# Performance work log

Measured on AMD Instinct MI355X. Metric: run time of the kernel, lower is better.

The kernel has to match this reference:

```python
import jax, jax.numpy as jnp
import numpy as np

B, X, Y, T = 8, 256, 256, 64   # input grid; T == fno_width
MODES = 16
PAD = 8
T_LOOKBACK = 16
SCALE = 1.0 / (T * T_LOOKBACK)  # 1/(fno_width*t_lookback)


def setup_inputs() -> dict:
    key = jax.random.key(0)
    ks = jax.random.split(key, 5)
    m = MODES
    x = jax.random.normal(ks[0], (B, X, Y, T), dtype=jnp.float32)
    w_tl = SCALE * jax.random.uniform(ks[1], (m, m, m), dtype=jnp.float32)
    w_tr = SCALE * jax.random.uniform(ks[2], (m, m, m), dtype=jnp.float32)
    w_bl = SCALE * jax.random.uniform(ks[3], (m, m, m), dtype=jnp.float32)
    w_br = SCALE * jax.random.uniform(ks[4], (m, m, m), dtype=jnp.float32)
    z = jnp.zeros((m, m, m), dtype=jnp.float32)
    return {"x": x, "w_tl": w_tl, "w_tr": w_tr, "w_bl": w_bl, "w_br": w_br,
            "b_tl": z, "b_tr": z, "b_bl": z, "b_br": z}


def reference(x, w_tl, w_tr, w_bl, w_br, b_tl, b_tr, b_bl, b_br):
    m, pad = MODES, PAD
    # pad all three non-batch dims
    xp = jnp.pad(x, ((0, 0), (pad, pad), (pad, pad), (pad, pad)))
    # tf: x = complex(x, x); x_ft = real(fft3d(x)) == Re(F(a)) - Im(F(a))
    xc = jax.lax.complex(xp, xp)
    x_ft = jnp.real(jnp.fft.fftn(xc, axes=(1, 2, 3)))
    # four corner mode blocks along axes 1,2; low modes along axis 3
    m_tl = x_ft[:, :m, :m, :m]
    m_tr = x_ft[:, -m:, :m, :m]
    m_bl = x_ft[:, :m, -m:, :m]
    m_br = x_ft[:, -m:, -m:, :m]
    top = jnp.concatenate([m_tl * w_tl + b_tl, m_tr * w_tr + b_tr], axis=1)
    bot = jnp.concatenate([m_bl * w_bl + b_bl, m_br * w_br + b_br], axis=1)
    xwb = jnp.concatenate([top, bot], axis=2)  # [B, 2m, 2m, m]
    # pad back to the UNPADDED input shape (axes 1,2) and to fno_width (axis 3)
    xwb = jnp.pad(xwb, ((0, 0), (0, X - 2 * m), (0, Y - 2 * m), (0, T - m)))
    # tf: output = real(ifft3d(complex(xwb, xwb)))
    out = jnp.real(jnp.fft.ifftn(jax.lax.complex(xwb, xwb), axes=(1, 2, 3)))
    return out
```

## Files before the change

### kernel.cpp

```cpp
#include <hip/hip_runtime.h>

#define PI_D 3.141592653589793238462643383279502884


__global__ void k_tables(float2* __restrict__ wt, float2* __restrict__ vt,
                         float2* __restrict__ vxy,
                         float2* __restrict__ pqf, float2* __restrict__ pqi,
                         float2* __restrict__ t16, float2* __restrict__ t1) {
  int t = blockIdx.x * blockDim.x + threadIdx.x;
  if (t < 64 * 16) {
    int n3 = t >> 4, k3 = t & 15;
    int ph = (k3 * (n3 + 8)) % 80;
    double a = -2.0 * PI_D * (double)ph / 80.0;
    wt[t] = make_float2((float)cos(a), (float)sin(a));
  }
  if (t < 256 * 32) {
    int n = t >> 5, k = t & 31;
    int kk = (k < 16) ? k : (240 + k);
    int ph = (kk * (n + 8)) % 272;
    double a = -2.0 * PI_D * (double)ph / 272.0;
    double c = cos(a), s = sin(a);
    pqf[t] = make_float2((float)(c - s), (float)(-(c + s)));
  }
  if (t < 512) {
    int a = t >> 5, k = t & 31;
    int kk = (k < 16) ? k : (240 + k);
    int ph16 = (kk * 16 * a) % 272;
    double a16 = -2.0 * PI_D * (double)ph16 / 272.0;
    t16[t] = make_float2((float)cos(a16), (float)sin(a16));
    int ph1 = (kk * (a + 8)) % 272;
    double a1 = -2.0 * PI_D * (double)ph1 / 272.0;
    t1[t] = make_float2((float)cos(a1), (float)sin(a1));
  }
  if (t < 16 * 64) {
    int k3 = t >> 6, n3 = t & 63;
    int ph = (k3 * n3) & 63;
    double a = 2.0 * PI_D * (double)ph / 64.0;
    vt[t] = make_float2((float)cos(a), (float)sin(a));
  }
  if (t < 256 * 32) {
    int n = t >> 5, k = t & 31;
    int ph = (k * n) & 255;
    double a = 2.0 * PI_D * (double)ph / 256.0;
    double c = cos(a), s = sin(a);
    vxy[t] = make_float2((float)c, (float)s);
    const double inv = 1.0 / 4194304.0;
    pqi[t] = make_float2((float)((c - s) * inv), (float)((-(c + s)) * inv));
  }
}

__global__ __launch_bounds__(512, 6) void k_fwd(const float* __restrict__ x,
                                                float2* __restrict__ Bm,
                                                const float* __restrict__ wtf,
                                                const float2* __restrict__ t16,
                                                const float2* __restrict__ t1) {
  __shared__ float sX[16][260];
  __shared__ float sAt[256][36];
  int bn1 = blockIdx.x;
  int tid = threadIdx.x;
  int lane = tid & 63;
  int p = __builtin_amdgcn_readfirstlane(tid >> 6);
  const float4* xg = (const float4*)(x + (long)bn1 * 16384);
  const float* wrow = wtf + 4 * p;
  float2 acc[4][2];
#pragma unroll
  for (int i = 0; i < 4; i++) {
    acc[i][0] = make_float2(0.f, 0.f);
    acc[i][1] = make_float2(0.f, 0.f);
  }
  for (int Q = 0; Q < 4; Q++) {
    if (Q) __syncthreads();
#pragma unroll
    for (int e = 0; e < 2; e++) {
      int idx = tid + e * 512;
      int n2 = idx >> 2, qq = idx & 3;
      float4 v = xg[n2 * 16 + 4 * Q + qq];
      int cs = n2 ^ (qq * 4);
      sX[4 * qq + 0][cs] = v.x; sX[4 * qq + 1][cs] = v.y;
      sX[4 * qq + 2][cs] = v.z; sX[4 * qq + 3][cs] = v.w;
    }
    __syncthreads();
#pragma unroll
    for (int n3l = 0; n3l < 16; n3l++) {
      float4 xv = *(const float4*)&sX[n3l][(4 * lane) ^ ((n3l >> 2) * 4)];
      float4 w = *(const float4*)(wrow + (16 * Q + n3l) * 32);
      acc[0][0].x = fmaf(xv.x, w.x, acc[0][0].x); acc[0][0].y = fmaf(xv.x, w.y, acc[0][0].y);
      acc[0][1].x = fmaf(xv.x, w.z, acc[0][1].x); acc[0][1].y = fmaf(xv.x, w.w, acc[0][1].y);
      acc[1][0].x = fmaf(xv.y, w.x, acc[1][0].x); acc[1][0].y = fmaf(xv.y, w.y, acc[1][0].y);
      acc[1][1].x = fmaf(xv.y, w.z, acc[1][1].x); acc[1][1].y = fmaf(xv.y, w.w, acc[1][1].y);
      acc[2][0].x = fmaf(xv.z, w.x, acc[2][0].x); acc[2][0].y = fmaf(xv.z, w.y, acc[2][0].y);
      acc[2][1].x = fmaf(xv.z, w.z, acc[2][1].x); acc[2][1].y = fmaf(xv.z, w.w, acc[2][1].y);
      acc[3][0].x = fmaf(xv.w, w.x, acc[3][0].x); acc[3][0].y = fmaf(xv.w, w.y, acc[3][0].y);
      acc[3][1].x = fmaf(xv.w, w.z, acc[3][1].x); acc[3][1].y = fmaf(xv.w, w.w, acc[3][1].y);
    }
  }
#pragma unroll
  for (int i = 0; i < 4; i++) {
    *(float4*)&sAt[4 * lane + i][4 * p] =
        make_float4(acc[i][0].x, acc[i][0].y, acc[i][1].x, acc[i][1].y);
  }
  int k2 = lane & 31, s = lane >> 5;
  float2 W16[16], W1s[8];
#pragma unroll
  for (int a = 0; a < 16; a++) W16[a] = t16[a * 32 + k2];
#pragma unroll
  for (int u = 0; u < 8; u++) W1s[u] = t1[(2 * u + s) * 32 + k2];
  __syncthreads();
  {
    float2 a0 = make_float2(0.f, 0.f), a1 = make_float2(0.f, 0.f);
#pragma unroll
    for (int a = 0; a < 16; a++) {
      float2 wa = W16[a];
#pragma unroll
      for (int u = 0; u < 8; u++) {
        int n2 = 16 * a + 2 * u + s;
        float4 av = *(const float4*)&sAt[n2][4 * p];
        float2 wb = W1s[u];
        float wx = fmaf(wa.x, wb.x, -wa.y * wb.y);
        float wy = fmaf(wa.x, wb.y, wa.y * wb.x);
        a0.x = fmaf(av.x, wx, fmaf(-av.y, wy, a0.x));
        a0.y = fmaf(av.x, wy, fmaf(av.y, wx, a0.y));
        a1.x = fmaf(av.z, wx, fmaf(-av.w, wy, a1.x));
        a1.y = fmaf(av.z, wy, fmaf(av.w, wx, a1.y));
      }
    }
    a0.x += __shfl_xor(a0.x, 32); a0.y += __shfl_xor(a0.y, 32);
    a1.x += __shfl_xor(a1.x, 32); a1.y += __shfl_xor(a1.y, 32);
    if (s == 0) {
      *(float4*)&Bm[(long)bn1 * 512 + k2 * 16 + 2 * p] =
          make_float4(a0.x, a0.y, a1.x, a1.y);
    }
  }
}

__global__ __launch_bounds__(512, 2) void k_fft_x(
    const float2* __restrict__ Bm, float* __restrict__ y,
    const float2* __restrict__ pqf,
    const float* __restrict__ w_tl, const float* __restrict__ w_tr,
    const float* __restrict__ w_bl, const float* __restrict__ w_br,
    const float* __restrict__ b_tl, const float* __restrict__ b_tr,
    const float* __restrict__ b_bl, const float* __restrict__ b_br) {
  __shared__ float2 sB[4096];
  __shared__ float2 sPQ[8192];
  int b = blockIdx.x >> 5, k2 = blockIdx.x & 31;
  int tid = threadIdx.x;
  for (int i = tid; i < 4096; i += 512) {
    sB[i] = Bm[((long)(b * 256 + (i >> 4)) * 32 + k2) * 16 + (i & 15)];
  }
  const float4* pq4 = (const float4*)pqf;
  float4* sPQ4 = (float4*)sPQ;
#pragma unroll
  for (int e = 0; e < 8; e++) sPQ4[tid + e * 512] = pq4[tid + e * 512];
  __syncthreads();
  int k1 = tid >> 4, k3 = tid & 15;
  float acc = 0.f;
#pragma unroll 8
  for (int n1 = 0; n1 < 256; n1++) {
    float2 a = sB[n1 * 16 + k3];
    float2 w = sPQ[n1 * 32 + k1];
    acc = fmaf(a.x, w.x, acc);
    acc = fmaf(a.y, w.y, acc);
  }
  const float* wsel = (k1 < 16) ? ((k2 < 16) ? w_tl : w_bl) : ((k2 < 16) ? w_tr : w_br);
  const float* bsel = (k1 < 16) ? ((k2 < 16) ? b_tl : b_bl) : ((k2 < 16) ? b_tr : b_br);
  int idx = ((k1 & 15) * 16 + (k2 & 15)) * 16 + k3;
  y[((b * 32 + k1) * 32 + k2) * 16 + k3] = fmaf(acc, wsel[idx], bsel[idx]);
}

__global__ __launch_bounds__(256, 2) void k_inv_te(const float* __restrict__ y,
                                                   float2* __restrict__ E,
                                                   const float2* __restrict__ vt,
                                                   const float2* __restrict__ vxy) {
  __shared__ float sy[512];
  __shared__ float2 svt[1024];
  __shared__ float sD[32][132];
  __shared__ float sV[128][66];
  int blk = blockIdx.x;
  int h = blk & 1, bk1 = blk >> 1;
  int tid = threadIdx.x;
  ((float2*)sy)[tid] = ((const float2*)(y + (long)bk1 * 512))[tid];
#pragma unroll
  for (int e = 0; e < 4; e++) svt[tid + e * 256] = vt[tid + e * 256];
#pragma unroll
  for (int e = 0; e < 16; e++) {
    int q = tid + e * 256;
    int n2l = q >> 5, k2 = q & 31;
    float2 v = vxy[(h * 128 + n2l) * 32 + k2];
    *(float2*)&sV[n2l][2 * k2] = v;
  }
  __syncthreads();
#pragma unroll
  for (int e = 0; e < 8; e++) {
    int idx = tid + e * 256;
    int k2 = idx >> 6, n3i = idx & 63;
    float ax = 0.f, ay = 0.f;
#pragma unroll
    for (int k3 = 0; k3 < 16; k3++) {
      float yv = sy[k2 * 16 + k3];
      float2 v = svt[k3 * 64 + n3i];
      ax = fmaf(yv, v.x, ax); ay = fmaf(yv, v.y, ay);
    }
    *(float2*)&sD[k2][2 * n3i] = make_float2(ax, ay);
  }
  __syncthreads();
  int rg = tid >> 3, tn = tid & 7;
  float acc[4][16];
#pragma unroll
  for (int i = 0; i < 4; i++)
#pragma unroll
    for (int j = 0; j < 16; j++) acc[i][j] = 0.f;
#pragma unroll 2
  for (int k2 = 0; k2 < 32; k2++) {
    float4 d0 = *(const float4*)&sD[k2][tn * 16];
    float4 d1 = *(const float4*)&sD[k2][tn * 16 + 4];
    float4 d2 = *(const float4*)&sD[k2][tn * 16 + 8];
    float4 d3 = *(const float4*)&sD[k2][tn * 16 + 12];
#pragma unroll
    for (int i = 0; i < 4; i++) {
      float2 v = *(const float2*)&sV[rg * 4 + i][2 * k2];
      float c = v.x, s = v.y;
      acc[i][0]  = fmaf(c, d0.x, fmaf(-s, d0.y, acc[i][0]));
      acc[i][1]  = fmaf(c, d0.y, fmaf( s, d0.x, acc[i][1]));
      acc[i][2]  = fmaf(c, d0.z, fmaf(-s, d0.w, acc[i][2]));
      acc[i][3]  = fmaf(c, d0.w, fmaf( s, d0.z, acc[i][3]));
      acc[i][4]  = fmaf(c, d1.x, fmaf(-s, d1.y, acc[i][4]));
      acc[i][5]  = fmaf(c, d1.y, fmaf( s, d1.x, acc[i][5]));
      acc[i][6]  = fmaf(c, d1.z, fmaf(-s, d1.w, acc[i][6]));
      acc[i][7]  = fmaf(c, d1.w, fmaf( s, d1.z, acc[i][7]));
      acc[i][8]  = fmaf(c, d2.x, fmaf(-s, d2.y, acc[i][8]));
      acc[i][9]  = fmaf(c, d2.y, fmaf( s, d2.x, acc[i][9]));
      acc[i][10] = fmaf(c, d2.z, fmaf(-s, d2.w, acc[i][10]));
      acc[i][11] = fmaf(c, d2.w, fmaf( s, d2.z, acc[i][11]));
      acc[i][12] = fmaf(c, d3.x, fmaf(-s, d3.y, acc[i][12]));
      acc[i][13] = fmaf(c, d3.y, fmaf( s, d3.x, acc[i][13]));
      acc[i][14] = fmaf(c, d3.z, fmaf(-s, d3.w, acc[i][14]));
      acc[i][15] = fmaf(c, d3.w, fmaf( s, d3.z, acc[i][15]));
    }
  }
#pragma unroll
  for (int i = 0; i < 4; i++) {
    int n2g = h * 128 + rg * 4 + i;
    float4* dst = (float4*)&E[((long)bk1 * 256 + n2g) * 64 + tn * 8];
    dst[0] = make_float4(acc[i][0], acc[i][1], acc[i][2], acc[i][3]);
    dst[1] = make_float4(acc[i][4], acc[i][5], acc[i][6], acc[i][7]);
    dst[2] = make_float4(acc[i][8], acc[i][9], acc[i][10], acc[i][11]);
    dst[3] = make_float4(acc[i][12], acc[i][13], acc[i][14], acc[i][15]);
  }
}

__global__ __launch_bounds__(256, 2) void k_ifft_x(const float2* __restrict__ E,
                                                   float* __restrict__ out,
                                                   const float2* __restrict__ pqi) {
  __shared__ float sW[64][256];
  __shared__ float sD[64][64];
  int blk = blockIdx.x;
  int tc = blk & 255, b = blk >> 8;
  int tid = threadIdx.x;
  {
    const float4* pq4 = (const float4*)pqi;
#pragma unroll
    for (int r = 0; r < 16; r++) {
      float4 v = pq4[tid * 16 + r];
      sW[4 * r][tid] = v.x; sW[4 * r + 1][tid] = v.y;
      sW[4 * r + 2][tid] = v.z; sW[4 * r + 3][tid] = v.w;
    }
  }
  {
    const float4* Eg = (const float4*)E;
#pragma unroll
    for (int e = 0; e < 2; e++) {
      int tq = tid + e * 256;
      int k1 = tq >> 4, cq = tq & 15;
      const float4* src = Eg + ((long)(b * 32 + k1) * 8192) + tc * 32 + 2 * cq;
      float4 v0 = src[0], v1 = src[1];
      *(float4*)&sD[2 * k1][4 * cq]     = make_float4(v0.x, v0.z, v1.x, v1.z);
      *(float4*)&sD[2 * k1 + 1][4 * cq] = make_float4(v0.y, v0.w, v1.y, v1.w);
    }
  }
  __syncthreads();
  int tm = tid >> 3, tn = tid & 7;
  float acc[8][8];
#pragma unroll
  for (int i = 0; i < 8; i++)
#pragma unroll
    for (int j = 0; j < 8; j++) acc[i][j] = 0.f;
#pragma unroll 2
  for (int kk = 0; kk < 64; kk++) {
    float4 wa = *(const float4*)&sW[kk][tm * 8];
    float4 wb = *(const float4*)&sW[kk][tm * 8 + 4];
    float4 da = *(const float4*)&sD[kk][tn * 8];
    float4 db = *(const float4*)&sD[kk][tn * 8 + 4];
    float w[8] = {wa.x, wa.y, wa.z, wa.w, wb.x, wb.y, wb.z, wb.w};
    float d[8] = {da.x, da.y, da.z, da.w, db.x, db.y, db.z, db.w};
#pragma unroll
    for (int i = 0; i < 8; i++)
#pragma unroll
      for (int j = 0; j < 8; j++) acc[i][j] = fmaf(w[i], d[j], acc[i][j]);
  }
  float* ob = out + (long)b * 4194304 + (long)(tm * 8) * 16384 + tc * 64 + tn * 8;
#pragma unroll
  for (int i = 0; i < 8; i++) {
    float4* o = (float4*)(ob + (long)i * 16384);
    o[0] = make_float4(acc[i][0], acc[i][1], acc[i][2], acc[i][3]);
    o[1] = make_float4(acc[i][4], acc[i][5], acc[i][6], acc[i][7]);
  }
}

extern "C" void kernel_launch(void* const* d_in, const int* in_sizes, int n_in,
                              void* d_out, int out_size, void* d_ws, size_t ws_size,
                              hipStream_t stream) {
  const float* x    = (const float*)d_in[0];
  const float* w_tl = (const float*)d_in[1];
  const float* w_tr = (const float*)d_in[2];
  const float* w_bl = (const float*)d_in[3];
  const float* w_br = (const float*)d_in[4];
  const float* b_tl = (const float*)d_in[5];
  const float* b_tr = (const float*)d_in[6];
  const float* b_bl = (const float*)d_in[7];
  const float* b_br = (const float*)d_in[8];
  float* out = (float*)d_out;
  char* ws = (char*)d_ws;

  float2* Bm  = (float2*)(ws + 0);
  float*  y   = (float*)(ws + 8388608);
  float2* E   = (float2*)(ws + 10485760);
  float2* WT  = (float2*)(ws + 44040192);
  float2* VT  = (float2*)(ws + 44048384);
  float2* VXY = (float2*)(ws + 44056576);
  float2* PQF = (float2*)(ws + 44122112);
  float2* PQI = (float2*)(ws + 44187648);
  float2* T16 = (float2*)(ws + 44253184);
  float2* T1  = (float2*)(ws + 44257280);

  k_tables<<<32, 256, 0, stream>>>(WT, VT, VXY, PQF, PQI, T16, T1);
  k_fwd<<<2048, 512, 0, stream>>>(x, Bm, (const float*)WT, T16, T1);
  k_fft_x<<<256, 512, 0, stream>>>(Bm, y, PQF, w_tl, w_tr, w_bl, w_br,
                                   b_tl, b_tr, b_bl, b_br);
  k_inv_te<<<512, 256, 0, stream>>>(y, E, VT, VXY);
  k_ifft_x<<<2048, 256, 0, stream>>>(E, out, PQI);
}
```

Before: 186.4 us.

## Remap k_fwd thread work and factor twiddle products in the y-DFT stage

Result: faster. 178.9 us (-4.0%).

```diff
diff --git a/kernel.cpp b/kernel.cpp
--- a/kernel.cpp
+++ b/kernel.cpp
@@ -49,25 +49,23 @@
   }
 }
 
-__global__ __launch_bounds__(512, 6) void k_fwd(const float* __restrict__ x,
+__global__ __launch_bounds__(512, 4) void k_fwd(const float* __restrict__ x,
                                                 float2* __restrict__ Bm,
                                                 const float* __restrict__ wtf,
                                                 const float2* __restrict__ t16,
                                                 const float2* __restrict__ t1) {
   __shared__ float sX[16][260];
-  __shared__ float sAt[256][36];
+  __shared__ float sA2[8][256][4];
   int bn1 = blockIdx.x;
   int tid = threadIdx.x;
   int lane = tid & 63;
-  int p = __builtin_amdgcn_readfirstlane(tid >> 6);
+  int wv = __builtin_amdgcn_readfirstlane(tid >> 6);
+  int g = wv >> 1, h = wv & 1;
+  int n2own = g * 64 + lane;
   const float4* xg = (const float4*)(x + (long)bn1 * 16384);
-  const float* wrow = wtf + 4 * p;
-  float2 acc[4][2];
-#pragma unroll
-  for (int i = 0; i < 4; i++) {
-    acc[i][0] = make_float2(0.f, 0.f);
-    acc[i][1] = make_float2(0.f, 0.f);
-  }
+  float2 a8[8];
+#pragma unroll
+  for (int q = 0; q < 8; q++) a8[q] = make_float2(0.f, 0.f);
   for (int Q = 0; Q < 4; Q++) {
     if (Q) __syncthreads();
 #pragma unroll
@@ -82,22 +80,24 @@
     __syncthreads();
 #pragma unroll
     for (int n3l = 0; n3l < 16; n3l++) {
-      float4 xv = *(const float4*)&sX[n3l][(4 * lane) ^ ((n3l >> 2) * 4)];
-      float4 w = *(const float4*)(wrow + (16 * Q + n3l) * 32);
-      acc[0][0].x = fmaf(xv.x, w.x, acc[0][0].x); acc[0][0].y = fmaf(xv.x, w.y, acc[0][0].y);
-      acc[0][1].x = fmaf(xv.x, w.z, acc[0][1].x); acc[0][1].y = fmaf(xv.x, w.w, acc[0][1].y);
-      acc[1][0].x = fmaf(xv.y, w.x, acc[1][0].x); acc[1][0].y = fmaf(xv.y, w.y, acc[1][0].y);
-      acc[1][1].x = fmaf(xv.y, w.z, acc[1][1].x); acc[1][1].y = fmaf(xv.y, w.w, acc[1][1].y);
-      acc[2][0].x = fmaf(xv.z, w.x, acc[2][0].x); acc[2][0].y = fmaf(xv.z, w.y, acc[2][0].y);
-      acc[2][1].x = fmaf(xv.z, w.z, acc[2][1].x); acc[2][1].y = fmaf(xv.z, w.w, acc[2][1].y);
-      acc[3][0].x = fmaf(xv.w, w.x, acc[3][0].x); acc[3][0].y = fmaf(xv.w, w.y, acc[3][0].y);
-      acc[3][1].x = fmaf(xv.w, w.z, acc[3][1].x); acc[3][1].y = fmaf(xv.w, w.w, acc[3][1].y);
-    }
-  }
-#pragma unroll
-  for (int i = 0; i < 4; i++) {
-    *(float4*)&sAt[4 * lane + i][4 * p] =
-        make_float4(acc[i][0].x, acc[i][0].y, acc[i][1].x, acc[i][1].y);
+      float xv = sX[n3l][n2own ^ ((n3l >> 2) * 4)];
+      const float4* w4 = (const float4*)(wtf + (16 * Q + n3l) * 32 + h * 16);
+      float4 wA = w4[0], wB = w4[1], wC = w4[2], wD = w4[3];
+      a8[0].x = fmaf(xv, wA.x, a8[0].x); a8[0].y = fmaf(xv, wA.y, a8[0].y);
+      a8[1].x = fmaf(xv, wA.z, a8[1].x); a8[1].y = fmaf(xv, wA.w, a8[1].y);
+      a8[2].x = fmaf(xv, wB.x, a8[2].x); a8[2].y = fmaf(xv, wB.y, a8[2].y);
+      a8[3].x = fmaf(xv, wB.z, a8[3].x); a8[3].y = fmaf(xv, wB.w, a8[3].y);
+      a8[4].x = fmaf(xv, wC.x, a8[4].x); a8[4].y = fmaf(xv, wC.y, a8[4].y);
+      a8[5].x = fmaf(xv, wC.z, a8[5].x); a8[5].y = fmaf(xv, wC.w, a8[5].y);
+      a8[6].x = fmaf(xv, wD.x, a8[6].x); a8[6].y = fmaf(xv, wD.y, a8[6].y);
+      a8[7].x = fmaf(xv, wD.z, a8[7].x); a8[7].y = fmaf(xv, wD.w, a8[7].y);
+    }
+  }
+#pragma unroll
+  for (int pp = 0; pp < 4; pp++) {
+    int p = h * 4 + pp;
+    *(float4*)&sA2[p][n2own][0] =
+        make_float4(a8[2 * pp].x, a8[2 * pp].y, a8[2 * pp + 1].x, a8[2 * pp + 1].y);
   }
   int k2 = lane & 31, s = lane >> 5;
   float2 W16[16], W1s[8];
@@ -107,28 +107,32 @@
   for (int u = 0; u < 8; u++) W1s[u] = t1[(2 * u + s) * 32 + k2];
   __syncthreads();
   {
-    float2 a0 = make_float2(0.f, 0.f), a1 = make_float2(0.f, 0.f);
+    int p = wv;
+    float2 A0 = make_float2(0.f, 0.f), A1 = make_float2(0.f, 0.f);
 #pragma unroll
     for (int a = 0; a < 16; a++) {
-      float2 wa = W16[a];
+      float2 S0 = make_float2(0.f, 0.f), S1 = make_float2(0.f, 0.f);
 #pragma unroll
       for (int u = 0; u < 8; u++) {
         int n2 = 16 * a + 2 * u + s;
-        float4 av = *(const float4*)&sAt[n2][4 * p];
+        float4 av = *(const float4*)&sA2[p][n2][0];
         float2 wb = W1s[u];
-        float wx = fmaf(wa.x, wb.x, -wa.y * wb.y);
-        float wy = fmaf(wa.x, wb.y, wa.y * wb.x);
-        a0.x = fmaf(av.x, wx, fmaf(-av.y, wy, a0.x));
-        a0.y = fmaf(av.x, wy, fmaf(av.y, wx, a0.y));
-        a1.x = fmaf(av.z, wx, fmaf(-av.w, wy, a1.x));
-        a1.y = fmaf(av.z, wy, fmaf(av.w, wx, a1.y));
+        S0.x = fmaf(av.x, wb.x, fmaf(-av.y, wb.y, S0.x));
+        S0.y = fmaf(av.x, wb.y, fmaf(av.y, wb.x, S0.y));
+        S1.x = fmaf(av.z, wb.x, fmaf(-av.w, wb.y, S1.x));
+        S1.y = fmaf(av.z, wb.y, fmaf(av.w, wb.x, S1.y));
       }
-    }
-    a0.x += __shfl_xor(a0.x, 32); a0.y += __shfl_xor(a0.y, 32);
-    a1.x += __shfl_xor(a1.x, 32); a1.y += __shfl_xor(a1.y, 32);
+      float2 wa = W16[a];
+      A0.x = fmaf(S0.x, wa.x, fmaf(-S0.y, wa.y, A0.x));
+      A0.y = fmaf(S0.x, wa.y, fmaf(S0.y, wa.x, A0.y));
+      A1.x = fmaf(S1.x, wa.x, fmaf(-S1.y, wa.y, A1.x));
+      A1.y = fmaf(S1.x, wa.y, fmaf(S1.y, wa.x, A1.y));
+    }
+    A0.x += __shfl_xor(A0.x, 32); A0.y += __shfl_xor(A0.y, 32);
+    A1.x += __shfl_xor(A1.x, 32); A1.y += __shfl_xor(A1.y, 32);
     if (s == 0) {
       *(float4*)&Bm[(long)bn1 * 512 + k2 * 16 + 2 * p] =
-          make_float4(a0.x, a0.y, a1.x, a1.y);
+          make_float4(A0.x, A0.y, A1.x, A1.y);
     }
   }
 }
```
